# Performance work log

Hardware: AMD Instinct MI355X
Metric: run time of the kernel (lower is better)

## Reference

```python
import jax, jax.numpy as jnp
import numpy as np

N_NODES = 100000
N_EDGES = 1600000
IN_D = 128
H_D = 128
OUT_D = 128
N_GRAPHS = 64


def _linear_params(key, fan_in, fan_out):
    k1, k2 = jax.random.split(key)
    bound = 1.0 / np.sqrt(fan_in)
    w = jax.random.uniform(k1, (fan_in, fan_out), jnp.float32, -bound, bound)
    b = jax.random.uniform(k2, (fan_out,), jnp.float32, -bound, bound)
    return w, b


def setup_inputs() -> dict:
    key = jax.random.key(0)
    ks = jax.random.split(key, 16)
    x = jax.random.normal(ks[0], (N_NODES, IN_D), jnp.float32)
    edge_index = jax.random.randint(ks[1], (2, N_EDGES), 0, N_NODES, jnp.int64)
    batch = jnp.sort(jax.random.randint(ks[2], (N_NODES,), 0, N_GRAPHS, jnp.int64))
    w1_1, b1_1 = _linear_params(ks[3], IN_D, H_D)
    w2_1, b2_1 = _linear_params(ks[4], H_D, H_D)
    w1_2, b1_2 = _linear_params(ks[5], H_D, H_D)
    w2_2, b2_2 = _linear_params(ks[6], H_D, H_D)
    w1_3, b1_3 = _linear_params(ks[7], H_D, H_D)
    w2_3, b2_3 = _linear_params(ks[8], H_D, OUT_D)
    return {
        "x": x, "edge_index": edge_index, "batch": batch,
        "w1_1": w1_1, "b1_1": b1_1, "w2_1": w2_1, "b2_1": b2_1,
        "w1_2": w1_2, "b1_2": b1_2, "w2_2": w2_2, "b2_2": b2_2,
        "w1_3": w1_3, "b1_3": b1_3, "w2_3": w2_3, "b2_3": b2_3,
    }


def _gin_conv(x, src, dst, w1, b1, w2, b2):
    # sum-aggregate source features onto destination nodes, eps=0 -> add self
    agg = jax.ops.segment_sum(x[src], dst, num_segments=N_NODES)
    h = agg + x
    # MLP: Linear -> ReLU -> Linear
    h = jnp.maximum(h @ w1 + b1, 0.0) @ w2 + b2
    return h


def reference(x, edge_index, batch,
              w1_1, b1_1, w2_1, b2_1,
              w1_2, b1_2, w2_2, b2_2,
              w1_3, b1_3, w2_3, b2_3):
    src, dst = edge_index[0], edge_index[1]
    h = jax.nn.relu(_gin_conv(x, src, dst, w1_1, b1_1, w2_1, b2_1))
    h = jax.nn.relu(_gin_conv(h, src, dst, w1_2, b1_2, w2_2, b2_2))
    h = _gin_conv(h, src, dst, w1_3, b1_3, w2_3, b2_3)
    # global mean pool over graphs, then flatten
    sums = jax.ops.segment_sum(h, batch, num_segments=N_GRAPHS)
    counts = jax.ops.segment_sum(jnp.ones((h.shape[0],), h.dtype), batch, num_segments=N_GRAPHS)
    pooled = sums / jnp.maximum(counts, 1.0)[:, None]
    return pooled.reshape(-1)
```

## Files before the change

kernel.cpp:

```cpp
#include <hip/hip_runtime.h>

#define D 128
#define NB_E 512

typedef __attribute__((ext_vector_type(8))) short bf16x8;
typedef __attribute__((ext_vector_type(16))) float f32x16;

__device__ inline float b2f(unsigned int hi16_as_lo) {
  union { unsigned int u; float f; } v;
  v.u = hi16_as_lo;
  return v.f;
}
__device__ inline unsigned short f2b(float f) {
  union { float f; unsigned int u; } v;
  v.f = f;
  unsigned int r = v.u + 0x7FFFu + ((v.u >> 16) & 1u);
  return (unsigned short)(r >> 16);
}
__device__ inline unsigned int pk2(float lo, float hi) {
  return (unsigned int)f2b(lo) | ((unsigned int)f2b(hi) << 16);
}

__global__ __launch_bounds__(256) void convert_kernel(
    const float* __restrict__ in, unsigned short* __restrict__ out, int n8) {
  int i = blockIdx.x * 256 + threadIdx.x;
  if (i >= n8) return;
  const float4 a = *reinterpret_cast<const float4*>(in + (size_t)i * 8);
  const float4 b = *reinterpret_cast<const float4*>(in + (size_t)i * 8 + 4);
  unsigned short o[8] = {f2b(a.x), f2b(a.y), f2b(a.z), f2b(a.w),
                         f2b(b.x), f2b(b.y), f2b(b.z), f2b(b.w)};
  *reinterpret_cast<bf16x8*>(out + (size_t)i * 8) =
      *reinterpret_cast<bf16x8*>(o);
}

__global__ __launch_bounds__(256) void pack_w6_kernel(
    const float* __restrict__ w0, const float* __restrict__ w1,
    const float* __restrict__ w2, const float* __restrict__ w3,
    const float* __restrict__ w4, const float* __restrict__ w5,
    unsigned short* __restrict__ Wp) {
  const int m = blockIdx.x >> 3;
  const float* W = m == 0 ? w0
                 : m == 1 ? w1
                 : m == 2 ? w2
                 : m == 3 ? w3
                 : m == 4 ? w4
                          : w5;
  const int idx = (blockIdx.x & 7) * 256 + threadIdx.x;
  const int l = idx & 63;
  const int s = (idx >> 6) & 7;
  const int t = idx >> 9;
  const int n = (t << 5) + (l & 31);
  const int k0 = (s << 4) + ((l >> 5) << 3);
  unsigned short o[8];
#pragma unroll
  for (int i = 0; i < 8; ++i) o[i] = f2b(W[(size_t)(k0 + i) * D + n]);
  *reinterpret_cast<bf16x8*>(Wp + (size_t)m * 16384 + (size_t)idx * 8) =
      *reinterpret_cast<bf16x8*>(o);
}

__global__ __launch_bounds__(256) void bktA_kernel(
    const int* __restrict__ dst, int* __restrict__ bcount, int n_edges,
    int NBU, int epb) {
  __shared__ int cnt[512];
  for (int i = threadIdx.x; i < NBU; i += 256) cnt[i] = 0;
  __syncthreads();
  const int e0 = blockIdx.x * epb;
  const int e1 = min(e0 + epb, n_edges);
  for (int e = e0 + threadIdx.x; e < e1; e += 256)
    atomicAdd(&cnt[dst[e] >> 8], 1);
  __syncthreads();
  int* out = bcount + (size_t)blockIdx.x * NBU;
  for (int i = threadIdx.x; i < NBU; i += 256) out[i] = cnt[i];
}

__global__ __launch_bounds__(256) void bktB_kernel(
    const int* __restrict__ bcount, int* __restrict__ boff,
    int* __restrict__ btot, int NBU) {
  __shared__ int lds[256];
  const int j = blockIdx.x;
  const int t = threadIdx.x;
  const int a = bcount[(size_t)(2 * t) * NBU + j];
  const int b = bcount[(size_t)(2 * t + 1) * NBU + j];
  const int s = a + b;
  lds[t] = s;
  __syncthreads();
#pragma unroll
  for (int off = 1; off < 256; off <<= 1) {
    int p = 0;
    if (t >= off) p = lds[t - off];
    __syncthreads();
    lds[t] += p;
    __syncthreads();
  }
  const int excl = lds[t] - s;
  boff[(size_t)(2 * t) * NBU + j] = excl;
  boff[(size_t)(2 * t + 1) * NBU + j] = excl + a;
  if (t == 255) btot[j] = lds[255];
}

__global__ __launch_bounds__(256) void bktBase_kernel(
    const int* __restrict__ btot, int* __restrict__ base, int NBU) {
  __shared__ int lds[256];
  const int t = threadIdx.x;
  const int a = (2 * t < NBU) ? btot[2 * t] : 0;
  const int b = (2 * t + 1 < NBU) ? btot[2 * t + 1] : 0;
  const int s = a + b;
  lds[t] = s;
  __syncthreads();
#pragma unroll
  for (int off = 1; off < 256; off <<= 1) {
    int p = 0;
    if (t >= off) p = lds[t - off];
    __syncthreads();
    lds[t] += p;
    __syncthreads();
  }
  const int excl = lds[t] - s;
  if (2 * t <= NBU) base[2 * t] = excl;
  if (2 * t + 1 <= NBU) base[2 * t + 1] = excl + a;
}

__global__ __launch_bounds__(256) void bktC_kernel(
    const int* __restrict__ src, const int* __restrict__ dst,
    const int* __restrict__ boff, const int* __restrict__ base,
    unsigned int* __restrict__ ebuf, int n_edges, int NBU, int epb) {
  __shared__ int cur[512];
  const int* bo = boff + (size_t)blockIdx.x * NBU;
  for (int i = threadIdx.x; i < NBU; i += 256) cur[i] = base[i] + bo[i];
  __syncthreads();
  const int e0 = blockIdx.x * epb;
  const int e1 = min(e0 + epb, n_edges);
  for (int e = e0 + threadIdx.x; e < e1; e += 256) {
    const int d = dst[e];
    const int pos = atomicAdd(&cur[d >> 8], 1);
    ebuf[pos] = ((unsigned int)(d & 255) << 17) | (unsigned int)src[e];
  }
}

__global__ __launch_bounds__(256) void bktD_kernel(
    const unsigned int* __restrict__ ebuf, const int* __restrict__ base,
    int* __restrict__ rowptr, int* __restrict__ col, int n_nodes) {
  __shared__ int hist[256];
  __shared__ int lds[256];
  __shared__ int cursor[256];
  const int j = blockIdx.x;
  const int t = threadIdx.x;
  hist[t] = 0;
  __syncthreads();
  const int e0 = base[j], e1 = base[j + 1];
  for (int e = e0 + t; e < e1; e += 256)
    atomicAdd(&hist[ebuf[e] >> 17], 1);
  __syncthreads();
  const int h = hist[t];
  lds[t] = h;
  __syncthreads();
#pragma unroll
  for (int off = 1; off < 256; off <<= 1) {
    int p = 0;
    if (t >= off) p = lds[t - off];
    __syncthreads();
    lds[t] += p;
    __syncthreads();
  }
  const int excl = lds[t] - h;
  const int node = (j << 8) + t;
  if (node <= n_nodes) rowptr[node] = e0 + excl;
  cursor[t] = e0 + excl;
  __syncthreads();
  for (int e = e0 + t; e < e1; e += 256) {
    const unsigned int v = ebuf[e];
    const int pos = atomicAdd(&cursor[v >> 17], 1);
    col[pos] = (int)(v & 0x1FFFFu);
  }
}

__global__ __launch_bounds__(256) void gather_bf16_kernel(
    const unsigned short* __restrict__ X, const int* __restrict__ rowptr,
    const int* __restrict__ col, unsigned short* __restrict__ out,
    int n_nodes) {
  const int t = blockIdx.x * 256 + threadIdx.x;
  const int g = t >> 5;
  if (g >= n_nodes) return;
  const int c = t & 15;
  const int slot = (t >> 4) & 1;
  const uint4* Xv = reinterpret_cast<const uint4*>(X);
  float a0 = 0.f, a1 = 0.f, a2 = 0.f, a3 = 0.f;
  float a4 = 0.f, a5 = 0.f, a6 = 0.f, a7 = 0.f;
  if (slot == 0) {
    const uint4 u = Xv[(size_t)g * 16 + c];
    a0 = b2f(u.x << 16); a1 = b2f(u.x & 0xffff0000u);
    a2 = b2f(u.y << 16); a3 = b2f(u.y & 0xffff0000u);
    a4 = b2f(u.z << 16); a5 = b2f(u.z & 0xffff0000u);
    a6 = b2f(u.w << 16); a7 = b2f(u.w & 0xffff0000u);
  }
  const int beg = rowptr[g], end = rowptr[g + 1];
  int j = beg + slot;
  for (; j + 6 < end; j += 8) {
    const int s0 = col[j + 0];
    const int s1 = col[j + 2];
    const int s2 = col[j + 4];
    const int s3 = col[j + 6];
    const uint4 w0 = Xv[(size_t)s0 * 16 + c];
    const uint4 w1 = Xv[(size_t)s1 * 16 + c];
    const uint4 w2 = Xv[(size_t)s2 * 16 + c];
    const uint4 w3 = Xv[(size_t)s3 * 16 + c];
    a0 += b2f(w0.x << 16); a1 += b2f(w0.x & 0xffff0000u);
    a2 += b2f(w0.y << 16); a3 += b2f(w0.y & 0xffff0000u);
    a4 += b2f(w0.z << 16); a5 += b2f(w0.z & 0xffff0000u);
    a6 += b2f(w0.w << 16); a7 += b2f(w0.w & 0xffff0000u);
    a0 += b2f(w1.x << 16); a1 += b2f(w1.x & 0xffff0000u);
    a2 += b2f(w1.y << 16); a3 += b2f(w1.y & 0xffff0000u);
    a4 += b2f(w1.z << 16); a5 += b2f(w1.z & 0xffff0000u);
    a6 += b2f(w1.w << 16); a7 += b2f(w1.w & 0xffff0000u);
    a0 += b2f(w2.x << 16); a1 += b2f(w2.x & 0xffff0000u);
    a2 += b2f(w2.y << 16); a3 += b2f(w2.y & 0xffff0000u);
    a4 += b2f(w2.z << 16); a5 += b2f(w2.z & 0xffff0000u);
    a6 += b2f(w2.w << 16); a7 += b2f(w2.w & 0xffff0000u);
    a0 += b2f(w3.x << 16); a1 += b2f(w3.x & 0xffff0000u);
    a2 += b2f(w3.y << 16); a3 += b2f(w3.y & 0xffff0000u);
    a4 += b2f(w3.z << 16); a5 += b2f(w3.z & 0xffff0000u);
    a6 += b2f(w3.w << 16); a7 += b2f(w3.w & 0xffff0000u);
  }
  for (; j < end; j += 2) {
    const uint4 w = Xv[(size_t)col[j] * 16 + c];
    a0 += b2f(w.x << 16); a1 += b2f(w.x & 0xffff0000u);
    a2 += b2f(w.y << 16); a3 += b2f(w.y & 0xffff0000u);
    a4 += b2f(w.z << 16); a5 += b2f(w.z & 0xffff0000u);
    a6 += b2f(w.w << 16); a7 += b2f(w.w & 0xffff0000u);
  }
  a0 += __shfl_xor(a0, 16, 64);
  a1 += __shfl_xor(a1, 16, 64);
  a2 += __shfl_xor(a2, 16, 64);
  a3 += __shfl_xor(a3, 16, 64);
  a4 += __shfl_xor(a4, 16, 64);
  a5 += __shfl_xor(a5, 16, 64);
  a6 += __shfl_xor(a6, 16, 64);
  a7 += __shfl_xor(a7, 16, 64);
  if (slot == 0) {
    uint4 o;
    o.x = pk2(a0, a1);
    o.y = pk2(a2, a3);
    o.z = pk2(a4, a5);
    o.w = pk2(a6, a7);
    reinterpret_cast<uint4*>(out)[(size_t)g * 16 + c] = o;
  }
}

template <int RELU>
__global__ __launch_bounds__(512) void mlp2_kernel(
    const unsigned short* __restrict__ X, const unsigned short* __restrict__ Wp1,
    const unsigned short* __restrict__ Wp2, const float* __restrict__ bias1,
    const float* __restrict__ bias2, unsigned short* __restrict__ out,
    int n_strips) {
  __shared__ unsigned short wl1[16384];
  __shared__ unsigned short wl2[16384];
  __shared__ float bl1[128], bl2[128];

  const int lx = threadIdx.x & 63;
  const int wid = threadIdx.x >> 6;
  const int h = lx >> 5;
  const int nl = lx & 31;
  const int wg = blockIdx.x * 8 + wid;
  const int NW = gridDim.x * 8;
  const int s0 = (int)(((long long)wg * n_strips) / NW);
  const int s1 = (int)(((long long)(wg + 1) * n_strips) / NW);
  const int strip = s0;
  const bool active = (s0 < s1);

  bf16x8 xf[8];
  if (active) {
    const unsigned short* xrow = X + (size_t)(strip * 32 + nl) * D + h * 8;
#pragma unroll
    for (int s = 0; s < 8; ++s)
      xf[s] = *reinterpret_cast<const bf16x8*>(xrow + s * 16);
  }

  for (int i = threadIdx.x * 8; i < 16384; i += 512 * 8) {
    *reinterpret_cast<bf16x8*>(wl1 + i) = *reinterpret_cast<const bf16x8*>(Wp1 + i);
    *reinterpret_cast<bf16x8*>(wl2 + i) = *reinterpret_cast<const bf16x8*>(Wp2 + i);
  }
  if (threadIdx.x < 128) {
    bl1[threadIdx.x] = bias1[threadIdx.x];
    bl2[threadIdx.x] = bias2[threadIdx.x];
  }
  __syncthreads();
  if (!active) return;

  f32x16 acc1[4];
#pragma unroll
  for (int t1 = 0; t1 < 4; ++t1)
#pragma unroll
    for (int r = 0; r < 16; ++r)
      acc1[t1][r] = bl1[32 * t1 + (r & 3) + 8 * (r >> 2) + 4 * h];
#pragma unroll
  for (int s = 0; s < 8; ++s) {
#pragma unroll
    for (int t1 = 0; t1 < 4; ++t1) {
      const bf16x8 wf = *reinterpret_cast<const bf16x8*>(
          wl1 + ((t1 * 8 + s) * 64 + lx) * 8);
      acc1[t1] =
          __builtin_amdgcn_mfma_f32_32x32x16_bf16(wf, xf[s], acc1[t1], 0, 0, 0);
    }
  }

  f32x16 acc2[4];
#pragma unroll
  for (int t = 0; t < 4; ++t)
#pragma unroll
    for (int r = 0; r < 16; ++r)
      acc2[t][r] = bl2[32 * t + (r & 3) + 8 * (r >> 2) + 4 * h];
#pragma unroll
  for (int s2 = 0; s2 < 8; ++s2) {
    const int t1 = s2 >> 1;
    const int ro = (s2 & 1) << 3;
    const float g0 = fmaxf(acc1[t1][ro + 0], 0.f);
    const float g1 = fmaxf(acc1[t1][ro + 1], 0.f);
    const float g2 = fmaxf(acc1[t1][ro + 2], 0.f);
    const float g3 = fmaxf(acc1[t1][ro + 3], 0.f);
    const float g4 = fmaxf(acc1[t1][ro + 4], 0.f);
    const float g5 = fmaxf(acc1[t1][ro + 5], 0.f);
    const float g6 = fmaxf(acc1[t1][ro + 6], 0.f);
    const float g7 = fmaxf(acc1[t1][ro + 7], 0.f);
    const unsigned int pA0 = pk2(g0, g1), pA1 = pk2(g2, g3);
    const unsigned int pB0 = pk2(g4, g5), pB1 = pk2(g6, g7);
    const unsigned int sA0 = (unsigned int)__shfl((int)pA0, lx ^ 32, 64);
    const unsigned int sA1 = (unsigned int)__shfl((int)pA1, lx ^ 32, 64);
    const unsigned int sB0 = (unsigned int)__shfl((int)pB0, lx ^ 32, 64);
    const unsigned int sB1 = (unsigned int)__shfl((int)pB1, lx ^ 32, 64);
    union { unsigned int u[4]; bf16x8 v; } fr;
    fr.u[0] = h ? sB0 : pA0;
    fr.u[1] = h ? sB1 : pA1;
    fr.u[2] = h ? pB0 : sA0;
    fr.u[3] = h ? pB1 : sA1;
#pragma unroll
    for (int t = 0; t < 4; ++t) {
      const bf16x8 wf = *reinterpret_cast<const bf16x8*>(
          wl2 + ((t * 8 + s2) * 64 + lx) * 8);
      acc2[t] =
          __builtin_amdgcn_mfma_f32_32x32x16_bf16(wf, fr.v, acc2[t], 0, 0, 0);
    }
  }

  unsigned short* orow = out + (size_t)(strip * 32 + nl) * D + h * 8;
#pragma unroll
  for (int s = 0; s < 8; ++s) {
    const int t = s >> 1;
    const int ro = (s & 1) << 3;
    float g0 = acc2[t][ro + 0], g1 = acc2[t][ro + 1];
    float g2 = acc2[t][ro + 2], g3 = acc2[t][ro + 3];
    float g4 = acc2[t][ro + 4], g5 = acc2[t][ro + 5];
    float g6 = acc2[t][ro + 6], g7 = acc2[t][ro + 7];
    if (RELU) {
      g0 = fmaxf(g0, 0.f); g1 = fmaxf(g1, 0.f);
      g2 = fmaxf(g2, 0.f); g3 = fmaxf(g3, 0.f);
      g4 = fmaxf(g4, 0.f); g5 = fmaxf(g5, 0.f);
      g6 = fmaxf(g6, 0.f); g7 = fmaxf(g7, 0.f);
    }
    const unsigned int pA0 = pk2(g0, g1), pA1 = pk2(g2, g3);
    const unsigned int pB0 = pk2(g4, g5), pB1 = pk2(g6, g7);
    const unsigned int sA0 = (unsigned int)__shfl((int)pA0, lx ^ 32, 64);
    const unsigned int sA1 = (unsigned int)__shfl((int)pA1, lx ^ 32, 64);
    const unsigned int sB0 = (unsigned int)__shfl((int)pB0, lx ^ 32, 64);
    const unsigned int sB1 = (unsigned int)__shfl((int)pB1, lx ^ 32, 64);
    union { unsigned int u[4]; bf16x8 v; } fr;
    fr.u[0] = h ? sB0 : pA0;
    fr.u[1] = h ? sB1 : pA1;
    fr.u[2] = h ? pB0 : sA0;
    fr.u[3] = h ? pB1 : sA1;
    *reinterpret_cast<bf16x8*>(orow + s * 16) = fr.v;
  }
}

#define POOL_NODES_PER_GROUP 128

__global__ __launch_bounds__(256) void pool_kernel(
    const unsigned short* __restrict__ H, const int* __restrict__ batch,
    float* __restrict__ sums, float* __restrict__ counts, int n_nodes) {
  const int group = (blockIdx.x * 256 + threadIdx.x) >> 5;
  const int lane = threadIdx.x & 31;
  const int n0 = group * POOL_NODES_PER_GROUP;
  if (n0 >= n_nodes) return;
  const int n1 = min(n0 + POOL_NODES_PER_GROUP, n_nodes);
  const uint2* Hv = reinterpret_cast<const uint2*>(H);

  float a0 = 0.f, a1 = 0.f, a2 = 0.f, a3 = 0.f;
  int cur = batch[n0];
  int runlen = 0;
  for (int n = n0; n < n1; ++n) {
    const int g = batch[n];
    if (g != cur) {
      float* p = sums + (size_t)cur * D + lane * 4;
      unsafeAtomicAdd(p + 0, a0);
      unsafeAtomicAdd(p + 1, a1);
      unsafeAtomicAdd(p + 2, a2);
      unsafeAtomicAdd(p + 3, a3);
      if (lane == 0) unsafeAtomicAdd(counts + cur, (float)runlen);
      a0 = a1 = a2 = a3 = 0.f;
      cur = g;
      runlen = 0;
    }
    const uint2 v = Hv[(size_t)n * 32 + lane];
    a0 += b2f(v.x << 16);
    a1 += b2f(v.x & 0xffff0000u);
    a2 += b2f(v.y << 16);
    a3 += b2f(v.y & 0xffff0000u);
    ++runlen;
  }
  float* p = sums + (size_t)cur * D + lane * 4;
  unsafeAtomicAdd(p + 0, a0);
  unsafeAtomicAdd(p + 1, a1);
  unsafeAtomicAdd(p + 2, a2);
  unsafeAtomicAdd(p + 3, a3);
  if (lane == 0) unsafeAtomicAdd(counts + cur, (float)runlen);
}

__global__ __launch_bounds__(256) void pool_norm_kernel(
    float* __restrict__ out, const float* __restrict__ counts, int n) {
  int i = blockIdx.x * 256 + threadIdx.x;
  if (i >= n) return;
  float cnt = counts[i / D];
  out[i] = out[i] / fmaxf(cnt, 1.0f);
}

extern "C" void kernel_launch(void* const* d_in, const int* in_sizes, int n_in,
                              void* d_out, int out_size, void* d_ws,
                              size_t ws_size, hipStream_t stream) {
  const float* x = (const float*)d_in[0];
  const int* ei = (const int*)d_in[1];
  const int* batch = (const int*)d_in[2];
  const float* B[6] = {(const float*)d_in[4],  (const float*)d_in[6],
                       (const float*)d_in[8],  (const float*)d_in[10],
                       (const float*)d_in[12], (const float*)d_in[14]};

  const int n_nodes = in_sizes[2];
  const int n_edges = in_sizes[1] / 2;
  const int n_graphs = out_size / D;
  const int* src = ei;
  const int* dst = ei + n_edges;

  const size_t matB = (size_t)n_nodes * D * sizeof(unsigned short);
  unsigned short* bufA = (unsigned short*)d_ws;
  unsigned short* bufB = (unsigned short*)((char*)d_ws + matB);
  unsigned short* bufC = (unsigned short*)((char*)d_ws + 2 * matB);
  unsigned short* wpack = (unsigned short*)((char*)d_ws + 3 * matB);
  int* rowptr = (int*)((char*)wpack + 6 * 16384 * sizeof(unsigned short));
  int* colidx = rowptr + (n_nodes + 1);
  unsigned int* ebuf = (unsigned int*)(colidx + n_edges);
  const int NBU = (n_nodes + 255) >> 8;
  int* bcount = (int*)(ebuf + n_edges);
  int* boff = bcount + (size_t)NB_E * NBU;
  int* btot = boff + (size_t)NB_E * NBU;
  int* base = btot + NBU;
  float* counts = (float*)(base + NBU + 2);

  const dim3 blk(256);
  const int gather_blocks = (int)(((long long)n_nodes * 32 + 255) / 256);
  const int pool_groups =
      (n_nodes + POOL_NODES_PER_GROUP - 1) / POOL_NODES_PER_GROUP;
  const int pool_blocks = (pool_groups * 32 + 255) / 256;
  const int n_strips = n_nodes / 32;
  const int mlp_grid = 512;
  const int epb = (n_edges + NB_E - 1) / NB_E;

  convert_kernel<<<(n_nodes * (D / 8) + 255) / 256, blk, 0, stream>>>(
      x, bufA, n_nodes * (D / 8));
  pack_w6_kernel<<<48, blk, 0, stream>>>(
      (const float*)d_in[3], (const float*)d_in[5], (const float*)d_in[7],
      (const float*)d_in[9], (const float*)d_in[11], (const float*)d_in[13],
      wpack);

  bktA_kernel<<<NB_E, blk, 0, stream>>>(dst, bcount, n_edges, NBU, epb);
  bktB_kernel<<<NBU, blk, 0, stream>>>(bcount, boff, btot, NBU);
  bktBase_kernel<<<1, blk, 0, stream>>>(btot, base, NBU);
  bktC_kernel<<<NB_E, blk, 0, stream>>>(src, dst, boff, base, ebuf, n_edges,
                                        NBU, epb);
  bktD_kernel<<<NBU, blk, 0, stream>>>(ebuf, base, rowptr, colidx, n_nodes);

  gather_bf16_kernel<<<gather_blocks, blk, 0, stream>>>(bufA, rowptr, colidx,
                                                        bufB, n_nodes);
  mlp2_kernel<1><<<mlp_grid, 512, 0, stream>>>(bufB, wpack + 0 * 16384,
                                               wpack + 1 * 16384, B[0], B[1],
                                               bufC, n_strips);
  gather_bf16_kernel<<<gather_blocks, blk, 0, stream>>>(bufC, rowptr, colidx,
                                                        bufB, n_nodes);
  mlp2_kernel<1><<<mlp_grid, 512, 0, stream>>>(bufB, wpack + 2 * 16384,
                                               wpack + 3 * 16384, B[2], B[3],
                                               bufA, n_strips);
  gather_bf16_kernel<<<gather_blocks, blk, 0, stream>>>(bufA, rowptr, colidx,
                                                        bufB, n_nodes);
  mlp2_kernel<0><<<mlp_grid, 512, 0, stream>>>(bufB, wpack + 4 * 16384,
                                               wpack + 5 * 16384, B[4], B[5],
                                               bufC, n_strips);

  hipMemsetAsync(d_out, 0, (size_t)out_size * sizeof(float), stream);
  hipMemsetAsync(counts, 0, (size_t)n_graphs * sizeof(float), stream);
  pool_kernel<<<pool_blocks, blk, 0, stream>>>(bufC, batch, (float*)d_out,
                                               counts, n_nodes);
  pool_norm_kernel<<<(out_size + 255) / 256, blk, 0, stream>>>((float*)d_out,
                                                               counts,
                                                               out_size);
}
```

Measured before the change: 354.8 us.

## Merge prep kernels, fold base scan into bucket kernels, single-pass pool

Merges the x conversion, weight packing and bucket counting into one prep launch. Removes the separate base-scan kernel by recomputing the small bucket-total scan inside bktC and bktD. Replaces the atomic pool, the two memsets and the normalize kernel with one per-graph kernel that binary-searches the sorted batch array and reduces in shared memory. The goal is fewer launches and no atomics, at the cost of redundant scans in every block and a reliance on batch being sorted.

```diff
diff --git a/kernel.cpp b/kernel.cpp
--- a/kernel.cpp
+++ b/kernel.cpp
@@ -20,57 +20,65 @@
 __device__ inline unsigned int pk2(float lo, float hi) {
   return (unsigned int)f2b(lo) | ((unsigned int)f2b(hi) << 16);
 }
-
-__global__ __launch_bounds__(256) void convert_kernel(
-    const float* __restrict__ in, unsigned short* __restrict__ out, int n8) {
-  int i = blockIdx.x * 256 + threadIdx.x;
-  if (i >= n8) return;
-  const float4 a = *reinterpret_cast<const float4*>(in + (size_t)i * 8);
-  const float4 b = *reinterpret_cast<const float4*>(in + (size_t)i * 8 + 4);
-  unsigned short o[8] = {f2b(a.x), f2b(a.y), f2b(a.z), f2b(a.w),
-                         f2b(b.x), f2b(b.y), f2b(b.z), f2b(b.w)};
-  *reinterpret_cast<bf16x8*>(out + (size_t)i * 8) =
-      *reinterpret_cast<bf16x8*>(o);
-}
-
-__global__ __launch_bounds__(256) void pack_w6_kernel(
+__device__ inline int lbound(const int* __restrict__ a, int n, int key) {
+  int lo = 0, hi = n;
+  while (lo < hi) {
+    int mid = (lo + hi) >> 1;
+    if (a[mid] < key) lo = mid + 1; else hi = mid;
+  }
+  return lo;
+}
+
+__global__ __launch_bounds__(256) void prep_kernel(
+    const float* __restrict__ x, unsigned short* __restrict__ xb,
     const float* __restrict__ w0, const float* __restrict__ w1,
     const float* __restrict__ w2, const float* __restrict__ w3,
     const float* __restrict__ w4, const float* __restrict__ w5,
-    unsigned short* __restrict__ Wp) {
-  const int m = blockIdx.x >> 3;
-  const float* W = m == 0 ? w0
-                 : m == 1 ? w1
-                 : m == 2 ? w2
-                 : m == 3 ? w3
-                 : m == 4 ? w4
-                          : w5;
-  const int idx = (blockIdx.x & 7) * 256 + threadIdx.x;
-  const int l = idx & 63;
-  const int s = (idx >> 6) & 7;
-  const int t = idx >> 9;
-  const int n = (t << 5) + (l & 31);
-  const int k0 = (s << 4) + ((l >> 5) << 3);
-  unsigned short o[8];
-#pragma unroll
-  for (int i = 0; i < 8; ++i) o[i] = f2b(W[(size_t)(k0 + i) * D + n]);
-  *reinterpret_cast<bf16x8*>(Wp + (size_t)m * 16384 + (size_t)idx * 8) =
-      *reinterpret_cast<bf16x8*>(o);
-}
-
-__global__ __launch_bounds__(256) void bktA_kernel(
-    const int* __restrict__ dst, int* __restrict__ bcount, int n_edges,
-    int NBU, int epb) {
+    unsigned short* __restrict__ Wp, const int* __restrict__ dst,
+    int* __restrict__ bcount, int n8, int n_edges, int NBU, int epb) {
   __shared__ int cnt[512];
-  for (int i = threadIdx.x; i < NBU; i += 256) cnt[i] = 0;
-  __syncthreads();
-  const int e0 = blockIdx.x * epb;
-  const int e1 = min(e0 + epb, n_edges);
-  for (int e = e0 + threadIdx.x; e < e1; e += 256)
-    atomicAdd(&cnt[dst[e] >> 8], 1);
-  __syncthreads();
-  int* out = bcount + (size_t)blockIdx.x * NBU;
-  for (int i = threadIdx.x; i < NBU; i += 256) out[i] = cnt[i];
+  const int b = blockIdx.x;
+  if (b < NB_E) {
+    for (int i = threadIdx.x; i < NBU; i += 256) cnt[i] = 0;
+    __syncthreads();
+    const int e0 = b * epb;
+    const int e1 = min(e0 + epb, n_edges);
+    for (int e = e0 + threadIdx.x; e < e1; e += 256)
+      atomicAdd(&cnt[dst[e] >> 8], 1);
+    __syncthreads();
+    int* out = bcount + (size_t)b * NBU;
+    for (int i = threadIdx.x; i < NBU; i += 256) out[i] = cnt[i];
+  } else if (b < NB_E + 48) {
+    const int bb = b - NB_E;
+    const int m = bb >> 3;
+    const float* W = m == 0 ? w0
+                   : m == 1 ? w1
+                   : m == 2 ? w2
+                   : m == 3 ? w3
+                   : m == 4 ? w4
+                            : w5;
+    const int idx = (bb & 7) * 256 + threadIdx.x;
+    const int l = idx & 63;
+    const int s = (idx >> 6) & 7;
+    const int t = idx >> 9;
+    const int n = (t << 5) + (l & 31);
+    const int k0 = (s << 4) + ((l >> 5) << 3);
+    unsigned short o[8];
+#pragma unroll
+    for (int i = 0; i < 8; ++i) o[i] = f2b(W[(size_t)(k0 + i) * D + n]);
+    *reinterpret_cast<bf16x8*>(Wp + (size_t)m * 16384 + (size_t)idx * 8) =
+        *reinterpret_cast<bf16x8*>(o);
+  } else {
+    const int i = (b - NB_E - 48) * 256 + threadIdx.x;
+    if (i < n8) {
+      const float4 a = *reinterpret_cast<const float4*>(x + (size_t)i * 8);
+      const float4 c = *reinterpret_cast<const float4*>(x + (size_t)i * 8 + 4);
+      unsigned short o[8] = {f2b(a.x), f2b(a.y), f2b(a.z), f2b(a.w),
+                             f2b(c.x), f2b(c.y), f2b(c.z), f2b(c.w)};
+      *reinterpret_cast<bf16x8*>(xb + (size_t)i * 8) =
+          *reinterpret_cast<bf16x8*>(o);
+    }
+  }
 }
 
 __global__ __launch_bounds__(256) void bktB_kernel(
@@ -98,39 +106,34 @@
   if (t == 255) btot[j] = lds[255];
 }
 
-__global__ __launch_bounds__(256) void bktBase_kernel(
-    const int* __restrict__ btot, int* __restrict__ base, int NBU) {
-  __shared__ int lds[256];
+__global__ __launch_bounds__(256) void bktC_kernel(
+    const int* __restrict__ src, const int* __restrict__ dst,
+    const int* __restrict__ boff, const int* __restrict__ btot,
+    unsigned int* __restrict__ ebuf, int n_edges, int NBU, int epb) {
+  __shared__ int cur[512];
+  __shared__ int scan[256];
   const int t = threadIdx.x;
   const int a = (2 * t < NBU) ? btot[2 * t] : 0;
   const int b = (2 * t + 1 < NBU) ? btot[2 * t + 1] : 0;
   const int s = a + b;
-  lds[t] = s;
+  scan[t] = s;
   __syncthreads();
 #pragma unroll
   for (int off = 1; off < 256; off <<= 1) {
     int p = 0;
-    if (t >= off) p = lds[t - off];
-    __syncthreads();
-    lds[t] += p;
-    __syncthreads();
-  }
-  const int excl = lds[t] - s;
-  if (2 * t <= NBU) base[2 * t] = excl;
-  if (2 * t + 1 <= NBU) base[2 * t + 1] = excl + a;
-}
-
-__global__ __launch_bounds__(256) void bktC_kernel(
-    const int* __restrict__ src, const int* __restrict__ dst,
-    const int* __restrict__ boff, const int* __restrict__ base,
-    unsigned int* __restrict__ ebuf, int n_edges, int NBU, int epb) {
-  __shared__ int cur[512];
+    if (t >= off) p = scan[t - off];
+    __syncthreads();
+    scan[t] += p;
+    __syncthreads();
+  }
+  const int excl = scan[t] - s;
   const int* bo = boff + (size_t)blockIdx.x * NBU;
-  for (int i = threadIdx.x; i < NBU; i += 256) cur[i] = base[i] + bo[i];
+  if (2 * t < NBU) cur[2 * t] = excl + bo[2 * t];
+  if (2 * t + 1 < NBU) cur[2 * t + 1] = excl + a + bo[2 * t + 1];
   __syncthreads();
   const int e0 = blockIdx.x * epb;
   const int e1 = min(e0 + epb, n_edges);
-  for (int e = e0 + threadIdx.x; e < e1; e += 256) {
+  for (int e = e0 + t; e < e1; e += 256) {
     const int d = dst[e];
     const int pos = atomicAdd(&cur[d >> 8], 1);
     ebuf[pos] = ((unsigned int)(d & 255) << 17) | (unsigned int)src[e];
@@ -138,16 +141,38 @@
 }
 
 __global__ __launch_bounds__(256) void bktD_kernel(
-    const unsigned int* __restrict__ ebuf, const int* __restrict__ base,
-    int* __restrict__ rowptr, int* __restrict__ col, int n_nodes) {
+    const unsigned int* __restrict__ ebuf, const int* __restrict__ btot,
+    int* __restrict__ rowptr, int* __restrict__ col, int n_nodes, int NBU) {
   __shared__ int hist[256];
   __shared__ int lds[256];
   __shared__ int cursor[256];
+  __shared__ int ebnd[2];
   const int j = blockIdx.x;
   const int t = threadIdx.x;
+  {
+    const int a = (2 * t < NBU) ? btot[2 * t] : 0;
+    const int b = (2 * t + 1 < NBU) ? btot[2 * t + 1] : 0;
+    const int s = a + b;
+    lds[t] = s;
+    __syncthreads();
+#pragma unroll
+    for (int off = 1; off < 256; off <<= 1) {
+      int p = 0;
+      if (t >= off) p = lds[t - off];
+      __syncthreads();
+      lds[t] += p;
+      __syncthreads();
+    }
+    const int excl = lds[t] - s;
+    if (2 * t == j) ebnd[0] = excl;
+    if (2 * t + 1 == j) ebnd[0] = excl + a;
+    if (2 * t == j + 1) ebnd[1] = excl;
+    if (2 * t + 1 == j + 1) ebnd[1] = excl + a;
+  }
+  __syncthreads();
+  const int e0 = ebnd[0], e1 = ebnd[1];
   hist[t] = 0;
   __syncthreads();
-  const int e0 = base[j], e1 = base[j + 1];
   for (int e = e0 + t; e < e1; e += 256)
     atomicAdd(&hist[ebuf[e] >> 17], 1);
   __syncthreads();
@@ -371,55 +396,50 @@
   }
 }
 
-#define POOL_NODES_PER_GROUP 128
-
-__global__ __launch_bounds__(256) void pool_kernel(
+__global__ __launch_bounds__(256) void pool1_kernel(
     const unsigned short* __restrict__ H, const int* __restrict__ batch,
-    float* __restrict__ sums, float* __restrict__ counts, int n_nodes) {
-  const int group = (blockIdx.x * 256 + threadIdx.x) >> 5;
-  const int lane = threadIdx.x & 31;
-  const int n0 = group * POOL_NODES_PER_GROUP;
-  if (n0 >= n_nodes) return;
-  const int n1 = min(n0 + POOL_NODES_PER_GROUP, n_nodes);
+    float* __restrict__ out, int n_nodes) {
+  __shared__ float red[256][4];
+  __shared__ int bnd[2];
+  const int g = blockIdx.x >> 2;
+  const int q = blockIdx.x & 3;
+  const int t = threadIdx.x;
+  if (t == 0) {
+    bnd[0] = lbound(batch, n_nodes, g);
+    bnd[1] = lbound(batch, n_nodes, g + 1);
+  }
+  __syncthreads();
+  const int start = bnd[0], end = bnd[1];
+  const int c = q * 8 + (t & 7);
   const uint2* Hv = reinterpret_cast<const uint2*>(H);
-
   float a0 = 0.f, a1 = 0.f, a2 = 0.f, a3 = 0.f;
-  int cur = batch[n0];
-  int runlen = 0;
-  for (int n = n0; n < n1; ++n) {
-    const int g = batch[n];
-    if (g != cur) {
-      float* p = sums + (size_t)cur * D + lane * 4;
-      unsafeAtomicAdd(p + 0, a0);
-      unsafeAtomicAdd(p + 1, a1);
-      unsafeAtomicAdd(p + 2, a2);
-      unsafeAtomicAdd(p + 3, a3);
-      if (lane == 0) unsafeAtomicAdd(counts + cur, (float)runlen);
-      a0 = a1 = a2 = a3 = 0.f;
-      cur = g;
-      runlen = 0;
-    }
-    const uint2 v = Hv[(size_t)n * 32 + lane];
+  for (int r = start + (t >> 3); r < end; r += 32) {
+    const uint2 v = Hv[(size_t)r * 32 + c];
     a0 += b2f(v.x << 16);
     a1 += b2f(v.x & 0xffff0000u);
     a2 += b2f(v.y << 16);
     a3 += b2f(v.y & 0xffff0000u);
-    ++runlen;
-  }
-  float* p = sums + (size_t)cur * D + lane * 4;
-  unsafeAtomicAdd(p + 0, a0);
-  unsafeAtomicAdd(p + 1, a1);
-  unsafeAtomicAdd(p + 2, a2);
-  unsafeAtomicAdd(p + 3, a3);
-  if (lane == 0) unsafeAtomicAdd(counts + cur, (float)runlen);
-}
-
-__global__ __launch_bounds__(256) void pool_norm_kernel(
-    float* __restrict__ out, const float* __restrict__ counts, int n) {
-  int i = blockIdx.x * 256 + threadIdx.x;
-  if (i >= n) return;
-  float cnt = counts[i / D];
-  out[i] = out[i] / fmaxf(cnt, 1.0f);
+  }
+  red[t][0] = a0;
+  red[t][1] = a1;
+  red[t][2] = a2;
+  red[t][3] = a3;
+  __syncthreads();
+#pragma unroll
+  for (int off = 16; off >= 1; off >>= 1) {
+    if ((t >> 3) < off) {
+#pragma unroll
+      for (int k = 0; k < 4; ++k) red[t][k] += red[t + off * 8][k];
+    }
+    __syncthreads();
+  }
+  if (t < 8) {
+    const float inv = 1.0f / (float)max(end - start, 1);
+    const int cc = q * 8 + t;
+#pragma unroll
+    for (int k = 0; k < 4; ++k)
+      out[(size_t)g * D + cc * 4 + k] = red[t][k] * inv;
+  }
 }
 
 extern "C" void kernel_launch(void* const* d_in, const int* in_sizes, int n_in,
@@ -450,31 +470,24 @@
   int* bcount = (int*)(ebuf + n_edges);
   int* boff = bcount + (size_t)NB_E * NBU;
   int* btot = boff + (size_t)NB_E * NBU;
-  int* base = btot + NBU;
-  float* counts = (float*)(base + NBU + 2);
 
   const dim3 blk(256);
   const int gather_blocks = (int)(((long long)n_nodes * 32 + 255) / 256);
-  const int pool_groups =
-      (n_nodes + POOL_NODES_PER_GROUP - 1) / POOL_NODES_PER_GROUP;
-  const int pool_blocks = (pool_groups * 32 + 255) / 256;
   const int n_strips = n_nodes / 32;
   const int mlp_grid = 512;
   const int epb = (n_edges + NB_E - 1) / NB_E;
-
-  convert_kernel<<<(n_nodes * (D / 8) + 255) / 256, blk, 0, stream>>>(
-      x, bufA, n_nodes * (D / 8));
-  pack_w6_kernel<<<48, blk, 0, stream>>>(
-      (const float*)d_in[3], (const float*)d_in[5], (const float*)d_in[7],
-      (const float*)d_in[9], (const float*)d_in[11], (const float*)d_in[13],
-      wpack);
-
-  bktA_kernel<<<NB_E, blk, 0, stream>>>(dst, bcount, n_edges, NBU, epb);
+  const int n8 = n_nodes * (D / 8);
+  const int prep_blocks = NB_E + 48 + (n8 + 255) / 256;
+
+  prep_kernel<<<prep_blocks, blk, 0, stream>>>(
+      x, bufA, (const float*)d_in[3], (const float*)d_in[5],
+      (const float*)d_in[7], (const float*)d_in[9], (const float*)d_in[11],
+      (const float*)d_in[13], wpack, dst, bcount, n8, n_edges, NBU, epb);
   bktB_kernel<<<NBU, blk, 0, stream>>>(bcount, boff, btot, NBU);
-  bktBase_kernel<<<1, blk, 0, stream>>>(btot, base, NBU);
-  bktC_kernel<<<NB_E, blk, 0, stream>>>(src, dst, boff, base, ebuf, n_edges,
+  bktC_kernel<<<NB_E, blk, 0, stream>>>(src, dst, boff, btot, ebuf, n_edges,
                                         NBU, epb);
-  bktD_kernel<<<NBU, blk, 0, stream>>>(ebuf, base, rowptr, colidx, n_nodes);
+  bktD_kernel<<<NBU, blk, 0, stream>>>(ebuf, btot, rowptr, colidx, n_nodes,
+                                       NBU);
 
   gather_bf16_kernel<<<gather_blocks, blk, 0, stream>>>(bufA, rowptr, colidx,
                                                         bufB, n_nodes);
@@ -492,11 +505,6 @@
                                                wpack + 5 * 16384, B[4], B[5],
                                                bufC, n_strips);
 
-  hipMemsetAsync(d_out, 0, (size_t)out_size * sizeof(float), stream);
-  hipMemsetAsync(counts, 0, (size_t)n_graphs * sizeof(float), stream);
-  pool_kernel<<<pool_blocks, blk, 0, stream>>>(bufC, batch, (float*)d_out,
-                                               counts, n_nodes);
-  pool_norm_kernel<<<(out_size + 255) / 256, blk, 0, stream>>>((float*)d_out,
-                                                               counts,
-                                                               out_size);
-}
+  pool1_kernel<<<n_graphs * 4, blk, 0, stream>>>(bufC, batch, (float*)d_out,
+                                                 n_nodes);
+}
```

New measurement: 311.5 us, median of 2. 12.2% less time.
